# Optimization experiments

Measured on AMD Instinct MI355X. Metric: run time of the kernel, lower is better.

## Reference

```python
import jax, jax.numpy as jnp
import numpy as np

N = 131072        # batch of spacetime points
IN_FEAT = 5       # modified spherical features
WIDTH = 128       # SmoothMLP width (config default)
DEPTH = 4         # hidden layers (config default); 1 input layer + 3 stacked hidden
CLIP = 1.0
EPS = 1e-8


def _init_mlp(key, in_dim, width, n_stack):
    ks = jax.random.split(key, 2 * (n_stack + 2))
    s_in = 1.0 / np.sqrt(in_dim)
    s_h = 1.0 / np.sqrt(width)
    W0 = jax.random.normal(ks[0], (in_dim, width), jnp.float32) * s_in
    b0 = jnp.zeros((width,), jnp.float32)
    Wh = jax.random.normal(ks[1], (n_stack, width, width), jnp.float32) * s_h
    bh = jnp.zeros((n_stack, width), jnp.float32)
    Wo = jax.random.normal(ks[2], (width, 1), jnp.float32) * s_h
    bo = jnp.zeros((1,), jnp.float32)
    return W0, b0, Wh, bh, Wo, bo


def setup_inputs() -> dict:
    key = jax.random.key(0)
    k_x, k_dp, k_ic = jax.random.split(key, 3)
    tx_cart = jax.random.normal(k_x, (N, 4), jnp.float32)
    # make times positive so the integration interval [0, t] is well posed
    tx_cart = tx_cart.at[:, 0].set(jnp.abs(tx_cart[:, 0]) + 0.1)
    dp = _init_mlp(k_dp, IN_FEAT + 1, WIDTH, DEPTH - 1)  # delta_phi net: [t, sph...]
    ic = _init_mlp(k_ic, IN_FEAT, WIDTH, DEPTH - 1)       # initial correction net
    names_dp = ["dp_W0", "dp_b0", "dp_Wh", "dp_bh", "dp_Wo", "dp_bo"]
    names_ic = ["ic_W0", "ic_b0", "ic_Wh", "ic_bh", "ic_Wo", "ic_bo"]
    out = {"tx_cart": tx_cart}
    out.update(dict(zip(names_dp, dp)))
    out.update(dict(zip(names_ic, ic)))
    return out


def _mlp(x, W0, b0, Wh, bh, Wo, bo):
    # SmoothMLP: tanh activations, scalar output. x: (..., in_dim)
    h = jnp.tanh(x @ W0 + b0)
    for i in range(Wh.shape[0]):  # fixed small layer count
        h = jnp.tanh(h @ Wh[i] + bh[i])
    return h @ Wo + bo  # (..., 1)


def _cart_to_mod_sph(x_cart):
    # Modified spherical coords with smooth radial compactification (clip):
    # [r/(clip+r), cos(theta), sin(theta), cos(phi), sin(phi)] -> 5 features
    x, y, z = x_cart[:, 0], x_cart[:, 1], x_cart[:, 2]
    r = jnp.sqrt(x * x + y * y + z * z + EPS)
    rho = jnp.sqrt(x * x + y * y + EPS)
    u = r / (CLIP + r)
    cos_t = z / r
    sin_t = rho / r
    cos_p = x / rho
    sin_p = y / rho
    return jnp.stack([u, cos_t, sin_t, cos_p, sin_p], axis=1)  # (N, 5)


# 3-point Gauss-Legendre nodes/weights on [-1, 1]
_GL_NODES = jnp.array([-np.sqrt(3.0 / 5.0), 0.0, np.sqrt(3.0 / 5.0)], jnp.float32)
_GL_WEIGHTS = jnp.array([5.0 / 9.0, 8.0 / 9.0, 5.0 / 9.0], jnp.float32)


def reference(tx_cart, dp_W0, dp_b0, dp_Wh, dp_bh, dp_Wo, dp_bo,
              ic_W0, ic_b0, ic_Wh, ic_bh, ic_Wo, ic_bo):
    t0 = 0.0
    t = tx_cart[:, 0]                        # (N,) per-row end time
    x_sph = _cart_to_mod_sph(tx_cart[:, 1:4])  # (N, 5)

    # initial correction at t0
    phi0 = _mlp(x_sph, ic_W0, ic_b0, ic_Wh, ic_bh, ic_Wo, ic_bo)[:, 0]  # (N,)

    # GL3 quadrature of d(phi)/dt over [t0, t] per row, fully vectorized
    a = (t - t0) * 0.5                       # (N,) half-width
    b = (t + t0) * 0.5                       # (N,) midpoint
    ts = a[:, None] * _GL_NODES[None, :] + b[:, None]          # (N, 3)
    sph_b = jnp.broadcast_to(x_sph[:, None, :], (x_sph.shape[0], 3, IN_FEAT))
    z = jnp.concatenate([ts[:, :, None], sph_b], axis=2)       # (N, 3, 6)
    vals = _mlp(z, dp_W0, dp_b0, dp_Wh, dp_bh, dp_Wo, dp_bo)[..., 0]  # (N, 3)
    delta_phi = a * jnp.sum(_GL_WEIGHTS * vals, axis=1)        # (N,)

    potential = phi0 + delta_phi
    return potential
```

## Files before the change

kernel.cpp:

```cpp
#include <hip/hip_runtime.h>

#define NPTS 131072
#define PPB  256
#define NBLK (NPTS / PPB)

#define FRAG0_OFF    0
#define FRAG0_BYTES  4096
#define FRAGH_OFF    4096
#define HLAYER_BYTES 32768
#define FRAGH_BYTES  (3 * HLAYER_BYTES)
#define BIAS_OFF     (FRAGH_OFF + FRAGH_BYTES)
#define BIAS_BYTES   2048
#define WO_OFF       (BIAS_OFF + BIAS_BYTES)
#define WOBO_BYTES   528
#define MLP_BYTES    (WO_OFF + WOBO_BYTES)

typedef _Float16 f16;
typedef __attribute__((ext_vector_type(8)))  _Float16 f16x8;
typedef __attribute__((ext_vector_type(16))) float    f32x16;

__device__ __forceinline__ float fast_tanh(float x){
  float e = __expf(2.0f * x);
  return 1.0f - 2.0f * __builtin_amdgcn_rcpf(e + 1.0f);
}

__global__ void pack_weights(
    const float* __restrict__ dpW0, const float* __restrict__ dpb0,
    const float* __restrict__ dpWh, const float* __restrict__ dpbh,
    const float* __restrict__ dpWo, const float* __restrict__ dpbo,
    const float* __restrict__ icW0, const float* __restrict__ icb0,
    const float* __restrict__ icWh, const float* __restrict__ icbh,
    const float* __restrict__ icWo, const float* __restrict__ icbo,
    unsigned char* __restrict__ ws)
{
  int tid = blockIdx.x * blockDim.x + threadIdx.x;
  int nth = gridDim.x * blockDim.x;
  for (int m = 0; m < 2; ++m){
    const float* W0 = m ? icW0 : dpW0;
    const float* Wh = m ? icWh : dpWh;
    const float* b0 = m ? icb0 : dpb0;
    const float* bh = m ? icbh : dpbh;
    const float* Wo = m ? icWo : dpWo;
    const float* bo = m ? icbo : dpbo;
    const int indim = m ? 5 : 6;
    unsigned char* base = ws + m * MLP_BYTES;

    f16* dstF0 = (f16*)(base + FRAG0_OFF);
    for (int idx = tid; idx < 2048; idx += nth){
      int e    = idx & 7;
      int lane = (idx >> 3) & 63;
      int jt   = idx >> 9;
      int j = 32*jt + (lane & 31);
      int k = 8*(lane >> 5) + e;
      float v = (k < indim) ? W0[k*128 + j] : 0.0f;
      dstF0[idx] = (f16)v;
    }
    f16* dstFH = (f16*)(base + FRAGH_OFF);
    for (int idx = tid; idx < 3*16384; idx += nth){
      int layer = idx / 16384;
      int q     = idx & 16383;
      int e    = q & 7;
      int lane = (q >> 3) & 63;
      int f    = q >> 9;
      int jt = f >> 3, s = f & 7;
      int j = 32*jt + (lane & 31);
      int k = 16*s + 8*(lane >> 5) + e;
      int row = (k & ~12) | ((k & 4) << 1) | ((k & 8) >> 1);
      float v = Wh[(layer*128 + row)*128 + j];
      dstFH[idx] = (f16)v;
    }
    float* dstB = (float*)(base + BIAS_OFF);
    for (int idx = tid; idx < 512; idx += nth)
      dstB[idx] = (idx < 128) ? b0[idx] : bh[idx - 128];
    float* dstW = (float*)(base + WO_OFF);
    for (int idx = tid; idx < 128; idx += nth) dstW[idx] = Wo[idx];
    if (tid == 0) dstW[128] = bo[0];
  }
}

__device__ __forceinline__ void stage_copy(const unsigned char* __restrict__ src,
                                           unsigned char* dst, int bytes, int tid){
  const uint4* s = (const uint4*)src;
  uint4* d = (uint4*)dst;
  const int n = bytes >> 4;
  for (int i = tid; i < n; i += 256) d[i] = s[i];
}

__launch_bounds__(256, 2)
__global__ void node_main(const float* __restrict__ tx,
                          const unsigned char* __restrict__ ws,
                          float* __restrict__ out)
{
  __shared__ __align__(16) unsigned char sFrag[HLAYER_BYTES];
  __shared__ __align__(16) float sBias[512];
  __shared__ __align__(16) float sWo[132];
  __shared__ float sVals[4][PPB];

  const int tid  = threadIdx.x;
  const int wave = tid >> 6;
  const int lane = tid & 63;
  const int p    = lane & 31;
  const int hi   = lane >> 5;
  const int blockBase = blockIdx.x * PPB;

  float u[2], cth[2], sth[2], cph[2], sph[2], th[2];
  #pragma unroll
  for (int ct = 0; ct < 2; ++ct){
    int gp = blockBase + wave*64 + ct*32 + p;
    float4 c = ((const float4*)tx)[gp];
    float x = c.y, y = c.z, z = c.w;
    float xy = x*x + y*y;
    float r   = sqrtf(xy + z*z + 1e-8f);
    float rho = sqrtf(xy + 1e-8f);
    float rin  = __builtin_amdgcn_rcpf(r);
    float rhin = __builtin_amdgcn_rcpf(rho);
    u[ct]   = r * __builtin_amdgcn_rcpf(1.0f + r);
    cth[ct] = z * rin;
    sth[ct] = rho * rin;
    cph[ct] = x * rhin;
    sph[ct] = y * rhin;
    th[ct]  = 0.5f * c.x;
  }

  f32x16 acc[4][2];

  auto bias_init = [&](int l){
    #pragma unroll
    for (int jt = 0; jt < 4; ++jt){
      const float* bp = &sBias[l*128 + 32*jt + 4*hi];
      float4 q0 = *(const float4*)(bp +  0);
      float4 q1 = *(const float4*)(bp +  8);
      float4 q2 = *(const float4*)(bp + 16);
      float4 q3 = *(const float4*)(bp + 24);
      f32x16 a;
      a[0]=q0.x;  a[1]=q0.y;  a[2]=q0.z;  a[3]=q0.w;
      a[4]=q1.x;  a[5]=q1.y;  a[6]=q1.z;  a[7]=q1.w;
      a[8]=q2.x;  a[9]=q2.y;  a[10]=q2.z; a[11]=q2.w;
      a[12]=q3.x; a[13]=q3.y; a[14]=q3.z; a[15]=q3.w;
      acc[jt][0] = a; acc[jt][1] = a;
    }
  };

  #pragma unroll 1
  for (int chain = 0; chain < 4; ++chain){
    const int mo = (chain == 3) ? MLP_BYTES : 0;
    __syncthreads();
    stage_copy(ws + mo + FRAG0_OFF, sFrag, FRAG0_BYTES, tid);
    if (chain == 0 || chain == 3){
      stage_copy(ws + mo + BIAS_OFF, (unsigned char*)sBias, BIAS_BYTES, tid);
      stage_copy(ws + mo + WO_OFF,   (unsigned char*)sWo,   WOBO_BYTES, tid);
    }
    const float gn = (chain == 0) ? -0.774596669241483f :
                     (chain == 2) ?  0.774596669241483f : 0.0f;

    f16x8 b0f[2];
    #pragma unroll
    for (int ct = 0; ct < 2; ++ct){
      #pragma unroll
      for (int e = 0; e < 8; ++e) b0f[ct][e] = (f16)0.0f;
      if (hi == 0){
        if (chain == 3){
          b0f[ct][0]=(f16)u[ct];   b0f[ct][1]=(f16)cth[ct];
          b0f[ct][2]=(f16)sth[ct]; b0f[ct][3]=(f16)cph[ct];
          b0f[ct][4]=(f16)sph[ct];
        } else {
          float ts = th[ct] * (1.0f + gn);
          b0f[ct][0]=(f16)ts;      b0f[ct][1]=(f16)u[ct];
          b0f[ct][2]=(f16)cth[ct]; b0f[ct][3]=(f16)sth[ct];
          b0f[ct][4]=(f16)cph[ct]; b0f[ct][5]=(f16)sph[ct];
        }
      }
    }
    __syncthreads();

    bias_init(0);
    {
      const f16x8* fr = (const f16x8*)sFrag;
      #pragma unroll
      for (int jt = 0; jt < 4; ++jt){
        f16x8 a = fr[jt*64 + lane];
        acc[jt][0] = __builtin_amdgcn_mfma_f32_32x32x16_f16(a, b0f[0], acc[jt][0], 0,0,0);
        acc[jt][1] = __builtin_amdgcn_mfma_f32_32x32x16_f16(a, b0f[1], acc[jt][1], 0,0,0);
      }
    }

    #pragma unroll 1
    for (int L = 0; L < 3; ++L){
      __syncthreads();
      stage_copy(ws + mo + FRAGH_OFF + L*HLAYER_BYTES, sFrag, HLAYER_BYTES, tid);
      f16x8 bf[2][8];
      #pragma unroll
      for (int ct = 0; ct < 2; ++ct)
        #pragma unroll
        for (int jt = 0; jt < 4; ++jt)
          #pragma unroll
          for (int c = 0; c < 2; ++c)
            #pragma unroll
            for (int e = 0; e < 8; ++e)
              bf[ct][2*jt + c][e] = (f16)fast_tanh(acc[jt][ct][8*c + e]);
      bias_init(L + 1);
      __syncthreads();
      const f16x8* fh = (const f16x8*)sFrag;
      #pragma unroll
      for (int jt = 0; jt < 4; ++jt)
        #pragma unroll
        for (int s = 0; s < 8; ++s){
          f16x8 a = fh[(jt*8 + s)*64 + lane];
          acc[jt][0] = __builtin_amdgcn_mfma_f32_32x32x16_f16(a, bf[0][s], acc[jt][0], 0,0,0);
          acc[jt][1] = __builtin_amdgcn_mfma_f32_32x32x16_f16(a, bf[1][s], acc[jt][1], 0,0,0);
        }
    }

    const float bo = sWo[128];
    #pragma unroll
    for (int ct = 0; ct < 2; ++ct){
      float v = 0.0f;
      #pragma unroll
      for (int jt = 0; jt < 4; ++jt){
        const float* wp = &sWo[32*jt + 4*hi];
        float4 q0 = *(const float4*)(wp +  0);
        float4 q1 = *(const float4*)(wp +  8);
        float4 q2 = *(const float4*)(wp + 16);
        float4 q3 = *(const float4*)(wp + 24);
        f32x16 A = acc[jt][ct];
        v += fast_tanh(A[0])*q0.x  + fast_tanh(A[1])*q0.y
           + fast_tanh(A[2])*q0.z  + fast_tanh(A[3])*q0.w
           + fast_tanh(A[4])*q1.x  + fast_tanh(A[5])*q1.y
           + fast_tanh(A[6])*q1.z  + fast_tanh(A[7])*q1.w
           + fast_tanh(A[8])*q2.x  + fast_tanh(A[9])*q2.y
           + fast_tanh(A[10])*q2.z + fast_tanh(A[11])*q2.w
           + fast_tanh(A[12])*q3.x + fast_tanh(A[13])*q3.y
           + fast_tanh(A[14])*q3.z + fast_tanh(A[15])*q3.w;
      }
      v += __shfl_xor(v, 32);
      v += bo;
      if (hi == 0) sVals[chain][wave*64 + ct*32 + p] = v;
    }
  }

  __syncthreads();
  {
    const int i  = tid;
    const int gp = blockBase + i;
    float t = tx[4*gp];
    float a = 0.5f * t;
    const float w13 = 0.5555555555555556f, w2 = 0.8888888888888889f;
    out[gp] = sVals[3][i] + a*(w13*sVals[0][i] + w2*sVals[1][i] + w13*sVals[2][i]);
  }
}

extern "C" void kernel_launch(void* const* d_in, const int* in_sizes, int n_in,
                              void* d_out, int out_size, void* d_ws, size_t ws_size,
                              hipStream_t stream)
{
  const float* tx = (const float*)d_in[0];
  pack_weights<<<64, 256, 0, stream>>>(
      (const float*)d_in[1],  (const float*)d_in[2],  (const float*)d_in[3],
      (const float*)d_in[4],  (const float*)d_in[5],  (const float*)d_in[6],
      (const float*)d_in[7],  (const float*)d_in[8],  (const float*)d_in[9],
      (const float*)d_in[10], (const float*)d_in[11], (const float*)d_in[12],
      (unsigned char*)d_ws);
  node_main<<<NBLK, 256, 0, stream>>>(tx, (const unsigned char*)d_ws, (float*)d_out);
}
```

Measured before the change: 101.8 us.

## Halve points per block, raise occupancy, use async global-to-LDS weight loads

Each wave now handles 32 points (one MFMA column tile) instead of 64, so blocks cover 128 points and the launch bound rises to 4 blocks per CU. Weight fragments are copied with global_load_lds straight into shared memory instead of through registers. The first-layer fragment gets its own buffer and is reloaded only per network. Other changes: bias is folded into the MFMA accumulator init, tanh uses exp2 with packed f16 conversion, and the quadrature sum is accumulated in registers instead of an sVals shared array. The trade is less weight reuse per block, since each weight fragment now feeds half as many points, for more resident waves to hide latency.

```diff
diff --git a/kernel.cpp b/kernel.cpp
--- a/kernel.cpp
+++ b/kernel.cpp
@@ -1,7 +1,7 @@
 #include <hip/hip_runtime.h>
 
 #define NPTS 131072
-#define PPB  256
+#define PPB  128
 #define NBLK (NPTS / PPB)
 
 #define FRAG0_OFF    0
@@ -19,9 +19,17 @@
 typedef __attribute__((ext_vector_type(8)))  _Float16 f16x8;
 typedef __attribute__((ext_vector_type(16))) float    f32x16;
 
-__device__ __forceinline__ float fast_tanh(float x){
-  float e = __expf(2.0f * x);
+#define C2LOG2E 2.8853900817779268f
+
+__device__ __forceinline__ float tanh_f(float x){
+  float e = __builtin_amdgcn_exp2f(x * C2LOG2E);
   return 1.0f - 2.0f * __builtin_amdgcn_rcpf(e + 1.0f);
+}
+
+__device__ __forceinline__ void gl_lds16(const void* g, void* l){
+  __builtin_amdgcn_global_load_lds(
+      (const __attribute__((address_space(1))) void*)g,
+      (__attribute__((address_space(3))) void*)l, 16, 0, 0);
 }
 
 __global__ void pack_weights(
@@ -78,175 +86,154 @@
   }
 }
 
-__device__ __forceinline__ void stage_copy(const unsigned char* __restrict__ src,
-                                           unsigned char* dst, int bytes, int tid){
-  const uint4* s = (const uint4*)src;
-  uint4* d = (uint4*)dst;
-  const int n = bytes >> 4;
-  for (int i = tid; i < n; i += 256) d[i] = s[i];
-}
-
-__launch_bounds__(256, 2)
+__device__ __forceinline__ f32x16 load_bias16(const float* bp){
+  float4 q0 = *(const float4*)(bp +  0);
+  float4 q1 = *(const float4*)(bp +  8);
+  float4 q2 = *(const float4*)(bp + 16);
+  float4 q3 = *(const float4*)(bp + 24);
+  f32x16 a;
+  a[0]=q0.x;  a[1]=q0.y;  a[2]=q0.z;  a[3]=q0.w;
+  a[4]=q1.x;  a[5]=q1.y;  a[6]=q1.z;  a[7]=q1.w;
+  a[8]=q2.x;  a[9]=q2.y;  a[10]=q2.z; a[11]=q2.w;
+  a[12]=q3.x; a[13]=q3.y; a[14]=q3.z; a[15]=q3.w;
+  return a;
+}
+
+__launch_bounds__(256, 4)
 __global__ void node_main(const float* __restrict__ tx,
                           const unsigned char* __restrict__ ws,
                           float* __restrict__ out)
 {
   __shared__ __align__(16) unsigned char sFrag[HLAYER_BYTES];
+  __shared__ __align__(16) unsigned char sF0[FRAG0_BYTES];
   __shared__ __align__(16) float sBias[512];
   __shared__ __align__(16) float sWo[132];
-  __shared__ float sVals[4][PPB];
 
   const int tid  = threadIdx.x;
   const int wave = tid >> 6;
   const int lane = tid & 63;
   const int p    = lane & 31;
   const int hi   = lane >> 5;
-  const int blockBase = blockIdx.x * PPB;
-
-  float u[2], cth[2], sth[2], cph[2], sph[2], th[2];
-  #pragma unroll
-  for (int ct = 0; ct < 2; ++ct){
-    int gp = blockBase + wave*64 + ct*32 + p;
-    float4 c = ((const float4*)tx)[gp];
-    float x = c.y, y = c.z, z = c.w;
-    float xy = x*x + y*y;
-    float r   = sqrtf(xy + z*z + 1e-8f);
-    float rho = sqrtf(xy + 1e-8f);
-    float rin  = __builtin_amdgcn_rcpf(r);
-    float rhin = __builtin_amdgcn_rcpf(rho);
-    u[ct]   = r * __builtin_amdgcn_rcpf(1.0f + r);
-    cth[ct] = z * rin;
-    sth[ct] = rho * rin;
-    cph[ct] = x * rhin;
-    sph[ct] = y * rhin;
-    th[ct]  = 0.5f * c.x;
-  }
-
-  f32x16 acc[4][2];
-
-  auto bias_init = [&](int l){
-    #pragma unroll
-    for (int jt = 0; jt < 4; ++jt){
-      const float* bp = &sBias[l*128 + 32*jt + 4*hi];
-      float4 q0 = *(const float4*)(bp +  0);
-      float4 q1 = *(const float4*)(bp +  8);
-      float4 q2 = *(const float4*)(bp + 16);
-      float4 q3 = *(const float4*)(bp + 24);
-      f32x16 a;
-      a[0]=q0.x;  a[1]=q0.y;  a[2]=q0.z;  a[3]=q0.w;
-      a[4]=q1.x;  a[5]=q1.y;  a[6]=q1.z;  a[7]=q1.w;
-      a[8]=q2.x;  a[9]=q2.y;  a[10]=q2.z; a[11]=q2.w;
-      a[12]=q3.x; a[13]=q3.y; a[14]=q3.z; a[15]=q3.w;
-      acc[jt][0] = a; acc[jt][1] = a;
-    }
-  };
+  const int gp   = blockIdx.x * PPB + wave * 32 + p;
+
+  float4 c = ((const float4*)tx)[gp];
+  float x = c.y, y = c.z, z = c.w;
+  float xy = x*x + y*y;
+  float r    = sqrtf(xy + z*z + 1e-8f);
+  float rho  = sqrtf(xy + 1e-8f);
+  float rin  = __builtin_amdgcn_rcpf(r);
+  float rhin = __builtin_amdgcn_rcpf(rho);
+  float u    = r * __builtin_amdgcn_rcpf(1.0f + r);
+  float cth  = z * rin;
+  float sth  = rho * rin;
+  float cph  = x * rhin;
+  float sph  = y * rhin;
+  float th   = 0.5f * c.x;
+
+  f32x16 acc[4];
+  float vsum = 0.0f;
 
   #pragma unroll 1
   for (int chain = 0; chain < 4; ++chain){
-    const int mo = (chain == 3) ? MLP_BYTES : 0;
-    __syncthreads();
-    stage_copy(ws + mo + FRAG0_OFF, sFrag, FRAG0_BYTES, tid);
+    const unsigned char* mb = ws + ((chain == 3) ? MLP_BYTES : 0);
+
     if (chain == 0 || chain == 3){
-      stage_copy(ws + mo + BIAS_OFF, (unsigned char*)sBias, BIAS_BYTES, tid);
-      stage_copy(ws + mo + WO_OFF,   (unsigned char*)sWo,   WOBO_BYTES, tid);
-    }
-    const float gn = (chain == 0) ? -0.774596669241483f :
-                     (chain == 2) ?  0.774596669241483f : 0.0f;
-
-    f16x8 b0f[2];
+      __syncthreads();
+      gl_lds16(mb + FRAG0_OFF + wave*1024 + lane*16, sF0 + wave*1024);
+      const uint4* s = (const uint4*)(mb + BIAS_OFF);
+      for (int i = tid; i < 128; i += 256) ((uint4*)sBias)[i] = s[i];
+      for (int i = tid; i < 33;  i += 256) ((uint4*)sWo)[i]   = s[128 + i];
+      __syncthreads();
+    }
+
+    const float gn = (chain == 0) ? -0.7745966692414834f :
+                     (chain == 2) ?  0.7745966692414834f : 0.0f;
+
+    f16x8 b0f;
     #pragma unroll
-    for (int ct = 0; ct < 2; ++ct){
+    for (int e = 0; e < 8; ++e) b0f[e] = (f16)0.0f;
+    if (hi == 0){
+      if (chain == 3){
+        b0f[0]=(f16)u;   b0f[1]=(f16)cth; b0f[2]=(f16)sth;
+        b0f[3]=(f16)cph; b0f[4]=(f16)sph;
+      } else {
+        float ts = th * (1.0f + gn);
+        b0f[0]=(f16)ts;  b0f[1]=(f16)u;   b0f[2]=(f16)cth;
+        b0f[3]=(f16)sth; b0f[4]=(f16)cph; b0f[5]=(f16)sph;
+      }
+    }
+
+    {
+      const f16x8* fr = (const f16x8*)sF0;
       #pragma unroll
-      for (int e = 0; e < 8; ++e) b0f[ct][e] = (f16)0.0f;
-      if (hi == 0){
-        if (chain == 3){
-          b0f[ct][0]=(f16)u[ct];   b0f[ct][1]=(f16)cth[ct];
-          b0f[ct][2]=(f16)sth[ct]; b0f[ct][3]=(f16)cph[ct];
-          b0f[ct][4]=(f16)sph[ct];
-        } else {
-          float ts = th[ct] * (1.0f + gn);
-          b0f[ct][0]=(f16)ts;      b0f[ct][1]=(f16)u[ct];
-          b0f[ct][2]=(f16)cth[ct]; b0f[ct][3]=(f16)sth[ct];
-          b0f[ct][4]=(f16)cph[ct]; b0f[ct][5]=(f16)sph[ct];
-        }
-      }
-    }
-    __syncthreads();
-
-    bias_init(0);
-    {
-      const f16x8* fr = (const f16x8*)sFrag;
-      #pragma unroll
-      for (int jt = 0; jt < 4; ++jt){
-        f16x8 a = fr[jt*64 + lane];
-        acc[jt][0] = __builtin_amdgcn_mfma_f32_32x32x16_f16(a, b0f[0], acc[jt][0], 0,0,0);
-        acc[jt][1] = __builtin_amdgcn_mfma_f32_32x32x16_f16(a, b0f[1], acc[jt][1], 0,0,0);
-      }
+      for (int jt = 0; jt < 4; ++jt)
+        acc[jt] = __builtin_amdgcn_mfma_f32_32x32x16_f16(
+                    fr[jt*64 + lane], b0f,
+                    load_bias16(&sBias[32*jt + 4*hi]), 0,0,0);
     }
 
     #pragma unroll 1
     for (int L = 0; L < 3; ++L){
       __syncthreads();
-      stage_copy(ws + mo + FRAGH_OFF + L*HLAYER_BYTES, sFrag, HLAYER_BYTES, tid);
-      f16x8 bf[2][8];
-      #pragma unroll
-      for (int ct = 0; ct < 2; ++ct)
+      {
+        const unsigned char* src = mb + FRAGH_OFF + L*HLAYER_BYTES + wave*8192;
+        unsigned char* dst = sFrag + wave*8192;
         #pragma unroll
-        for (int jt = 0; jt < 4; ++jt)
-          #pragma unroll
-          for (int c = 0; c < 2; ++c)
-            #pragma unroll
-            for (int e = 0; e < 8; ++e)
-              bf[ct][2*jt + c][e] = (f16)fast_tanh(acc[jt][ct][8*c + e]);
-      bias_init(L + 1);
-      __syncthreads();
-      const f16x8* fh = (const f16x8*)sFrag;
+        for (int i = 0; i < 8; ++i)
+          gl_lds16(src + i*1024 + lane*16, dst + i*1024);
+      }
+      union { f16x8 v; unsigned uu[4]; } bf[8];
       #pragma unroll
       for (int jt = 0; jt < 4; ++jt)
         #pragma unroll
-        for (int s = 0; s < 8; ++s){
-          f16x8 a = fh[(jt*8 + s)*64 + lane];
-          acc[jt][0] = __builtin_amdgcn_mfma_f32_32x32x16_f16(a, bf[0][s], acc[jt][0], 0,0,0);
-          acc[jt][1] = __builtin_amdgcn_mfma_f32_32x32x16_f16(a, bf[1][s], acc[jt][1], 0,0,0);
-        }
-    }
-
-    const float bo = sWo[128];
-    #pragma unroll
-    for (int ct = 0; ct < 2; ++ct){
-      float v = 0.0f;
+        for (int cq = 0; cq < 2; ++cq)
+          #pragma unroll
+          for (int e = 0; e < 4; ++e){
+            float t0 = tanh_f(acc[jt][8*cq + 2*e]);
+            float t1 = tanh_f(acc[jt][8*cq + 2*e + 1]);
+            auto pk = __builtin_amdgcn_cvt_pkrtz(t0, t1);
+            bf[2*jt + cq].uu[e] = __builtin_bit_cast(unsigned, pk);
+          }
+      __syncthreads();
+      const f16x8* fh = (const f16x8*)sFrag;
       #pragma unroll
       for (int jt = 0; jt < 4; ++jt){
-        const float* wp = &sWo[32*jt + 4*hi];
-        float4 q0 = *(const float4*)(wp +  0);
-        float4 q1 = *(const float4*)(wp +  8);
-        float4 q2 = *(const float4*)(wp + 16);
-        float4 q3 = *(const float4*)(wp + 24);
-        f32x16 A = acc[jt][ct];
-        v += fast_tanh(A[0])*q0.x  + fast_tanh(A[1])*q0.y
-           + fast_tanh(A[2])*q0.z  + fast_tanh(A[3])*q0.w
-           + fast_tanh(A[4])*q1.x  + fast_tanh(A[5])*q1.y
-           + fast_tanh(A[6])*q1.z  + fast_tanh(A[7])*q1.w
-           + fast_tanh(A[8])*q2.x  + fast_tanh(A[9])*q2.y
-           + fast_tanh(A[10])*q2.z + fast_tanh(A[11])*q2.w
-           + fast_tanh(A[12])*q3.x + fast_tanh(A[13])*q3.y
-           + fast_tanh(A[14])*q3.z + fast_tanh(A[15])*q3.w;
+        f32x16 t = load_bias16(&sBias[(L+1)*128 + 32*jt + 4*hi]);
+        #pragma unroll
+        for (int s = 0; s < 8; ++s)
+          t = __builtin_amdgcn_mfma_f32_32x32x16_f16(
+                fh[(jt*8 + s)*64 + lane], bf[s].v, t, 0,0,0);
+        acc[jt] = t;
       }
-      v += __shfl_xor(v, 32);
-      v += bo;
-      if (hi == 0) sVals[chain][wave*64 + ct*32 + p] = v;
-    }
+    }
+
+    float v = 0.0f;
+    #pragma unroll
+    for (int jt = 0; jt < 4; ++jt){
+      const float* wp = &sWo[32*jt + 4*hi];
+      float4 q0 = *(const float4*)(wp +  0);
+      float4 q1 = *(const float4*)(wp +  8);
+      float4 q2 = *(const float4*)(wp + 16);
+      float4 q3 = *(const float4*)(wp + 24);
+      f32x16 A = acc[jt];
+      v += tanh_f(A[0])*q0.x  + tanh_f(A[1])*q0.y
+         + tanh_f(A[2])*q0.z  + tanh_f(A[3])*q0.w
+         + tanh_f(A[4])*q1.x  + tanh_f(A[5])*q1.y
+         + tanh_f(A[6])*q1.z  + tanh_f(A[7])*q1.w
+         + tanh_f(A[8])*q2.x  + tanh_f(A[9])*q2.y
+         + tanh_f(A[10])*q2.z + tanh_f(A[11])*q2.w
+         + tanh_f(A[12])*q3.x + tanh_f(A[13])*q3.y
+         + tanh_f(A[14])*q3.z + tanh_f(A[15])*q3.w;
+    }
+    v += __shfl_xor(v, 32);
+    v += sWo[128];
+    const float coeff = (chain == 3) ? 1.0f
+                      : th * ((chain == 1) ? 0.8888888888888889f
+                                           : 0.5555555555555556f);
+    vsum = __builtin_fmaf(coeff, v, vsum);
   }
 
-  __syncthreads();
-  {
-    const int i  = tid;
-    const int gp = blockBase + i;
-    float t = tx[4*gp];
-    float a = 0.5f * t;
-    const float w13 = 0.5555555555555556f, w2 = 0.8888888888888889f;
-    out[gp] = sVals[3][i] + a*(w13*sVals[0][i] + w2*sVals[1][i] + w13*sVals[2][i]);
-  }
+  if (hi == 0) out[gp] = vsum;
 }
 
 extern "C" void kernel_launch(void* const* d_in, const int* in_sizes, int n_in,
```

After: 93.72 us. -8.0%, faster.
